# Performance work log

Hardware: AMD Instinct MI355X
Metric: run time of the kernel (lower is better)

Reference implementation:

```python
import jax, jax.numpy as jnp
import numpy as np

N = 50000      # nodes
E = 800000     # edges (before self-loops)
IN_F = 128     # in_feature
HID = 64       # hidden_feature (out_channels per head)
HEADS = 3
NEG_SLOPE = 0.2  # PyG GATConv default negative_slope


def setup_inputs() -> dict:
    key = jax.random.key(0)
    ks = jax.random.split(key, 12)
    x = jax.random.normal(ks[0], (N, IN_F), dtype=jnp.float32)
    src = jax.random.randint(ks[1], (E,), 0, N, dtype=jnp.int32)
    off = jax.random.randint(ks[2], (E,), 1, N, dtype=jnp.int32)
    dst = (src + off) % N  # guarantees no pre-existing self-loops
    edge_index = jnp.stack([src, dst]).astype(jnp.int32)

    def glorot(k, shape, fan_in):
        return (jax.random.normal(k, shape, dtype=jnp.float32)
                / np.float32(np.sqrt(fan_in)))

    W1 = glorot(ks[3], (IN_F, HEADS * HID), IN_F)
    att_src1 = glorot(ks[4], (HEADS, HID), HID)
    att_dst1 = glorot(ks[5], (HEADS, HID), HID)
    bias1 = jnp.zeros((HID,), jnp.float32)
    W2 = glorot(ks[6], (HID, HEADS * HID), HID)
    att_src2 = glorot(ks[7], (HEADS, HID), HID)
    att_dst2 = glorot(ks[8], (HEADS, HID), HID)
    bias2 = jnp.zeros((HID,), jnp.float32)
    return dict(x=x, edge_index=edge_index,
                W1=W1, att_src1=att_src1, att_dst1=att_dst1, bias1=bias1,
                W2=W2, att_src2=att_src2, att_dst2=att_dst2, bias2=bias2)


def gat_layer(x, W, a_src, a_dst, bias, src, dst):
    """PyG GATConv: heads=HEADS, concat=False (mean over heads), self-loops added."""
    h = (x @ W).reshape(-1, HEADS, HID)              # [N, H, C]
    alpha_src = jnp.einsum('nhc,hc->nh', h, a_src)   # [N, H]
    alpha_dst = jnp.einsum('nhc,hc->nh', h, a_dst)   # [N, H]
    loop = jnp.arange(N, dtype=src.dtype)
    s = jnp.concatenate([src, loop])                 # add self-loops
    d = jnp.concatenate([dst, loop])
    e = jax.nn.leaky_relu(alpha_src[s] + alpha_dst[d], NEG_SLOPE)  # [E+N, H]
    # segment softmax over edges grouped by destination node
    m = jax.ops.segment_max(e, d, num_segments=N)    # [N, H]; every node has a self-loop
    p = jnp.exp(e - m[d])
    denom = jax.ops.segment_sum(p, d, num_segments=N)
    alpha = p / (denom[d] + 1e-16)                   # [E+N, H]
    out = jax.ops.segment_sum(alpha[:, :, None] * h[s], d, num_segments=N)  # [N, H, C]
    return out.mean(axis=1) + bias                   # concat=False -> head mean


def reference(x, edge_index, W1, att_src1, att_dst1, bias1,
              W2, att_src2, att_dst2, bias2):
    src, dst = edge_index[0], edge_index[1]
    h1 = gat_layer(x, W1, att_src1, att_dst1, bias1, src, dst)
    h1 = jax.nn.relu(h1)  # dropout(p=0.2) is identity in eval mode
    return gat_layer(h1, W2, att_src2, att_dst2, bias2, src, dst)
```

## Files before the change

### kernel.cpp

```cpp
#include <hip/hip_runtime.h>
#include <hip/hip_fp16.h>
#include <math.h>
#include <limits.h>

#define N_NODES 50000
#define N_EDGES 800000
#define NEG 0.2f

typedef _Float16 half8 __attribute__((ext_vector_type(8)));
typedef float floatx4 __attribute__((ext_vector_type(4)));


__global__ void zero_kernel(int* a, int n) {
    int i = blockIdx.x * blockDim.x + threadIdx.x;
    if (i < n) a[i] = 0;
}

__global__ void count_kernel(const int* __restrict__ dst, int* cnt, int E) {
    int i = blockIdx.x * blockDim.x + threadIdx.x;
    if (i < E) atomicAdd(&cnt[dst[i]], 1);
}

__global__ void scan1_kernel(const int* __restrict__ cnt, int* rowptr, int* partials, int n) {
    __shared__ int sh[256];
    int tid = threadIdx.x;
    int i = blockIdx.x * 256 + tid;
    int v = (i < n) ? cnt[i] : 0;
    sh[tid] = v;
    __syncthreads();
    for (int off = 1; off < 256; off <<= 1) {
        int t = (tid >= off) ? sh[tid - off] : 0;
        __syncthreads();
        sh[tid] += t;
        __syncthreads();
    }
    if (i < n) rowptr[i] = sh[tid] - v;
    if (tid == 255) partials[blockIdx.x] = sh[255];
}

__global__ void scan2_kernel(int* partials, int nb) {
    __shared__ int sh[256];
    int tid = threadIdx.x;
    int v = (tid < nb) ? partials[tid] : 0;
    sh[tid] = v;
    __syncthreads();
    for (int off = 1; off < 256; off <<= 1) {
        int t = (tid >= off) ? sh[tid - off] : 0;
        __syncthreads();
        sh[tid] += t;
        __syncthreads();
    }
    if (tid < nb) partials[tid] = sh[tid] - v;
}

__global__ void scan3_kernel(int* rowptr, const int* __restrict__ partials, int n) {
    int i = blockIdx.x * blockDim.x + threadIdx.x;
    if (i < n) rowptr[i] += partials[i >> 8];
    if (i == 0) rowptr[n] = N_EDGES;
}

__global__ void fill_kernel(const int* __restrict__ src, const int* __restrict__ dst,
                            const int* __restrict__ rowptr, int* cnt, int* col, int* eidp, int E) {
    int i = blockIdx.x * blockDim.x + threadIdx.x;
    if (i < E) {
        int d = dst[i];
        int pos = rowptr[d] + atomicSub(&cnt[d], 1) - 1;
        col[pos] = src[i];
        eidp[pos] = i;
    }
}

__global__ void sortrow_kernel(const int* __restrict__ rowptr, int* col, int* eidp, int n) {
    int wid = (int)((blockIdx.x * blockDim.x + threadIdx.x) >> 6);
    int lane = threadIdx.x & 63;
    if (wid >= n) return;
    int r0 = rowptr[wid], r1 = rowptr[wid + 1];
    int deg = r1 - r0;
    if (deg <= 1) return;
    if (deg <= 64) {
        int key = (lane < deg) ? eidp[r0 + lane] : INT_MAX;
        int val = (lane < deg) ? col[r0 + lane] : 0;
#pragma unroll
        for (int k = 2; k <= 64; k <<= 1) {
#pragma unroll
            for (int j = k >> 1; j > 0; j >>= 1) {
                int pk = __shfl_xor(key, j);
                int pv = __shfl_xor(val, j);
                bool up = ((lane & k) == 0);
                bool lower = ((lane & j) == 0);
                bool take = lower ? ((pk < key) == up) : ((pk > key) == up);
                if (take) { key = pk; val = pv; }
            }
        }
        if (lane < deg) col[r0 + lane] = val;
    } else if (lane == 0) {
        for (int i = r0 + 1; i < r1; ++i) {
            int ke = eidp[i], kv = col[i];
            int j = i - 1;
            while (j >= r0 && eidp[j] > ke) {
                eidp[j + 1] = eidp[j];
                col[j + 1] = col[j];
                --j;
            }
            eidp[j + 1] = ke;
            col[j + 1] = kv;
        }
    }
}

template <int K>
__global__ void wtrans_kernel(const float* __restrict__ W, __half* __restrict__ wt) {
    int idx = blockIdx.x * blockDim.x + threadIdx.x;
    if (idx < 192 * K) {
        int n = idx / K, k = idx - n * K;
        wt[idx] = __float2half(W[k * 192 + n]);
    }
}

template <int K>
__global__ __launch_bounds__(256) void mfma_gemm_kernel(const float* __restrict__ A,
                                                        const __half* __restrict__ wt,
                                                        __half* __restrict__ out,
                                                        const float* __restrict__ att_src,
                                                        const float* __restrict__ att_dst,
                                                        float* __restrict__ as4,
                                                        float* __restrict__ ad4,
                                                        float* __restrict__ wself4, int rows) {
    constexpr int KP = K + 8;
    __shared__ __align__(16) __half lds[192 * KP];
    int tid = threadIdx.x;
    int lane = tid & 63;
    int wv = tid >> 6;
    int ln = lane & 15;
    int q = lane >> 4;

    for (int idx = tid; idx < 192 * (K / 8); idx += 256) {
        int n = idx / (K / 8), kk = (idx % (K / 8)) * 8;
        *(float4*)(lds + n * KP + kk) = *(const float4*)(wt + n * K + kk);
    }

    int m0 = blockIdx.x * 64 + wv * 16;
    int m = m0 + ln;
    int mc = m < rows ? m : 0;
    half8 afr[K / 32];
#pragma unroll
    for (int kt = 0; kt < K / 32; ++kt) {
        float4 a0 = *(const float4*)(A + (size_t)mc * K + kt * 32 + q * 8);
        float4 a1 = *(const float4*)(A + (size_t)mc * K + kt * 32 + q * 8 + 4);
        half8 f;
        f[0] = (_Float16)a0.x; f[1] = (_Float16)a0.y; f[2] = (_Float16)a0.z; f[3] = (_Float16)a0.w;
        f[4] = (_Float16)a1.x; f[5] = (_Float16)a1.y; f[6] = (_Float16)a1.z; f[7] = (_Float16)a1.w;
        afr[kt] = f;
    }

    __syncthreads();

    floatx4 acc[12];
#pragma unroll
    for (int c = 0; c < 12; ++c) acc[c] = (floatx4){0.f, 0.f, 0.f, 0.f};

#pragma unroll
    for (int kt = 0; kt < K / 32; ++kt) {
#pragma unroll
        for (int c = 0; c < 12; ++c) {
            half8 b = *(const half8*)(lds + (c * 16 + ln) * KP + kt * 32 + q * 8);
            acc[c] = __builtin_amdgcn_mfma_f32_16x16x32_f16(afr[kt], b, acc[c], 0, 0, 0);
        }
    }

    float asv[12], adv[12];
#pragma unroll
    for (int c = 0; c < 12; ++c) {
        asv[c] = att_src[c * 16 + ln];
        adv[c] = att_dst[c * 16 + ln];
    }
#pragma unroll
    for (int r = 0; r < 4; ++r) {
        float s0 = 0, s1 = 0, s2 = 0, d0 = 0, d1 = 0, d2 = 0;
#pragma unroll
        for (int c = 0; c < 4; ++c) { s0 += acc[c][r] * asv[c]; d0 += acc[c][r] * adv[c]; }
#pragma unroll
        for (int c = 4; c < 8; ++c) { s1 += acc[c][r] * asv[c]; d1 += acc[c][r] * adv[c]; }
#pragma unroll
        for (int c = 8; c < 12; ++c) { s2 += acc[c][r] * asv[c]; d2 += acc[c][r] * adv[c]; }
        for (int off = 1; off < 16; off <<= 1) {
            s0 += __shfl_xor(s0, off); s1 += __shfl_xor(s1, off); s2 += __shfl_xor(s2, off);
            d0 += __shfl_xor(d0, off); d1 += __shfl_xor(d1, off); d2 += __shfl_xor(d2, off);
        }
        int row = m0 + q * 4 + r;
        if (ln == 0 && row < rows) {
            as4[row * 4 + 0] = s0; as4[row * 4 + 1] = s1; as4[row * 4 + 2] = s2;
            ad4[row * 4 + 0] = d0; ad4[row * 4 + 1] = d1; ad4[row * 4 + 2] = d2;
            float v0 = s0 + d0; v0 = v0 > 0.f ? v0 : NEG * v0;
            float v1 = s1 + d1; v1 = v1 > 0.f ? v1 : NEG * v1;
            float v2 = s2 + d2; v2 = v2 > 0.f ? v2 : NEG * v2;
            wself4[row * 4 + 0] = __expf(v0);
            wself4[row * 4 + 1] = __expf(v1);
            wself4[row * 4 + 2] = __expf(v2);
        }
    }

    __syncthreads();
#pragma unroll
    for (int c = 0; c < 12; ++c)
#pragma unroll
        for (int r = 0; r < 4; ++r)
            lds[(wv * 16 + q * 4 + r) * 192 + c * 16 + ln] = __float2half(acc[c][r]);
    __syncthreads();
    int row0 = blockIdx.x * 64;
    for (int idx = tid; idx < 1536; idx += 256) {
        int row = (idx * 8) / 192, off = (idx * 8) % 192;
        if (row0 + row < rows)
            *(float4*)(out + (size_t)(row0 + row) * 192 + off) = *(float4*)(lds + row * 192 + off);
    }
}

template <bool RELU>
__global__ __launch_bounds__(256) void aggregate_kernel(const __half* __restrict__ h,
                                                        const float* __restrict__ as_,
                                                        const float* __restrict__ ad4,
                                                        const float* __restrict__ wself4,
                                                        const float* __restrict__ bias,
                                                        const int* __restrict__ rowptr,
                                                        const int* __restrict__ col,
                                                        float* __restrict__ out, int n) {
    constexpr int U = 8;
    __shared__ float sh[4][192];
    int wid = (int)((blockIdx.x * blockDim.x + threadIdx.x) >> 6);
    int l = threadIdx.x & 63;
    int wv = threadIdx.x >> 6;
    bool valid = wid < n;
    int d = valid ? wid : 0;
    if (valid && l < 48) {
        int hl = l >> 4;
        int r0 = rowptr[d], r1 = rowptr[d + 1];
        float adh = ad4[d * 4 + hl];
        float w = wself4[d * 4 + hl];
        float2 sraw = *(const float2*)(h + (size_t)d * 192 + l * 4);
        float2 s01 = __half22float2(*(__half2*)&sraw.x);
        float2 s23 = __half22float2(*(__half2*)&sraw.y);
        float ax = w * s01.x, ay = w * s01.y, az = w * s23.x, aw = w * s23.y;
        float den = w;

        for (int j = r0; j < r1; j += U) {
            int s[U];
            bool act[U];
            float av[U];
            float2 g[U];
#pragma unroll
            for (int u = 0; u < U; ++u) {
                int jj = j + u;
                act[u] = jj < r1;
                s[u] = act[u] ? col[jj] : 0;
            }
#pragma unroll
            for (int u = 0; u < U; ++u) {
                float t = as_[s[u] * 4 + hl];
                av[u] = act[u] ? t : -1e30f;
            }
#pragma unroll
            for (int u = 0; u < U; ++u)
                g[u] = *(const float2*)(h + (size_t)s[u] * 192 + l * 4);
#pragma unroll
            for (int u = 0; u < U; ++u) {
                float v = av[u] + adh;
                v = v > 0.f ? v : NEG * v;
                float we = __expf(v);
                float2 g01 = __half22float2(*(__half2*)&g[u].x);
                float2 g23 = __half22float2(*(__half2*)&g[u].y);
                den += we;
                ax += we * g01.x;
                ay += we * g01.y;
                az += we * g23.x;
                aw += we * g23.y;
            }
        }
        float r = 1.f / den;
        float4 o = {ax * r, ay * r, az * r, aw * r};
        *(float4*)&sh[wv][l * 4] = o;
    }
    __syncthreads();
    if (valid) {
        float o = (sh[wv][l] + sh[wv][64 + l] + sh[wv][128 + l]) * (1.f / 3.f) + bias[l];
        if (RELU) o = fmaxf(o, 0.f);
        out[(size_t)d * 64 + l] = o;
    }
}

extern "C" void kernel_launch(void* const* d_in, const int* in_sizes, int n_in,
                              void* d_out, int out_size, void* d_ws, size_t ws_size,
                              hipStream_t stream) {
    const float* x = (const float*)d_in[0];
    const int* ei = (const int*)d_in[1];
    const float* W1 = (const float*)d_in[2];
    const float* att_s1 = (const float*)d_in[3];
    const float* att_d1 = (const float*)d_in[4];
    const float* b1 = (const float*)d_in[5];
    const float* W2 = (const float*)d_in[6];
    const float* att_s2 = (const float*)d_in[7];
    const float* att_d2 = (const float*)d_in[8];
    const float* b2 = (const float*)d_in[9];
    const int* src = ei;
    const int* dst = ei + N_EDGES;

    __half* h16 = (__half*)d_ws;
    __half* wt1 = h16 + (size_t)N_NODES * 192;
    __half* wt2 = wt1 + 192 * 128;
    float* as4 = (float*)(wt2 + 192 * 64);
    float* ad4 = as4 + N_NODES * 4;
    float* wself4 = ad4 + N_NODES * 4;
    int* cnt = (int*)(wself4 + N_NODES * 4);
    int* rowptr = cnt + N_NODES;
    int* col = rowptr + N_NODES + 1;
    int* eidp = col + N_EDGES;
    int* partials = eidp + N_EDGES;

    float* outf = (float*)d_out;
    const int NB = (N_NODES + 255) / 256;

    wtrans_kernel<128><<<(192 * 128 + 255) / 256, 256, 0, stream>>>(W1, wt1);
    wtrans_kernel<64><<<(192 * 64 + 255) / 256, 256, 0, stream>>>(W2, wt2);

    zero_kernel<<<(N_NODES + 255) / 256, 256, 0, stream>>>(cnt, N_NODES);
    count_kernel<<<(N_EDGES + 255) / 256, 256, 0, stream>>>(dst, cnt, N_EDGES);
    scan1_kernel<<<NB, 256, 0, stream>>>(cnt, rowptr, partials, N_NODES);
    scan2_kernel<<<1, 256, 0, stream>>>(partials, NB);
    scan3_kernel<<<NB, 256, 0, stream>>>(rowptr, partials, N_NODES);
    fill_kernel<<<(N_EDGES + 255) / 256, 256, 0, stream>>>(src, dst, rowptr, cnt, col, eidp, N_EDGES);
    sortrow_kernel<<<(N_NODES + 3) / 4, 256, 0, stream>>>(rowptr, col, eidp, N_NODES);

    mfma_gemm_kernel<128><<<(N_NODES + 63) / 64, 256, 0, stream>>>(x, wt1, h16, att_s1, att_d1,
                                                                   as4, ad4, wself4, N_NODES);
    aggregate_kernel<true><<<(N_NODES + 3) / 4, 256, 0, stream>>>(h16, as4, ad4, wself4, b1,
                                                                  rowptr, col, outf, N_NODES);

    mfma_gemm_kernel<64><<<(N_NODES + 63) / 64, 256, 0, stream>>>(outf, wt2, h16, att_s2, att_d2,
                                                                  as4, ad4, wself4, N_NODES);
    aggregate_kernel<false><<<(N_NODES + 3) / 4, 256, 0, stream>>>(h16, as4, ad4, wself4, b2,
                                                                   rowptr, col, outf, N_NODES);
}
```

Measured before the change: 357.2 us.

## Streamline CSR build: store edge ids only, sort keys, then map to src

The CSR fill now writes only edge ids into col, using a cursor array that scan3 initializes, and the separate eidp array is dropped. The per-row bitonic sort then shuffles only keys and converts edge ids to source nodes at the end with a gathered load from src. Count and fill now process four edges per thread through int4 loads. This halves the scattered writes and shuffle traffic in the preprocessing stage, at the cost of an extra random gather from src during the sort.

```diff
diff --git a/kernel.cpp b/kernel.cpp
--- a/kernel.cpp
+++ b/kernel.cpp
@@ -17,8 +17,17 @@
 }
 
 __global__ void count_kernel(const int* __restrict__ dst, int* cnt, int E) {
-    int i = blockIdx.x * blockDim.x + threadIdx.x;
-    if (i < E) atomicAdd(&cnt[dst[i]], 1);
+    int t = blockIdx.x * blockDim.x + threadIdx.x;
+    int i0 = t * 4;
+    if (i0 + 3 < E) {
+        int4 d4 = *(const int4*)(dst + i0);
+        atomicAdd(&cnt[d4.x], 1);
+        atomicAdd(&cnt[d4.y], 1);
+        atomicAdd(&cnt[d4.z], 1);
+        atomicAdd(&cnt[d4.w], 1);
+    } else {
+        for (int i = i0; i < E; ++i) atomicAdd(&cnt[dst[i]], 1);
+    }
 }
 
 __global__ void scan1_kernel(const int* __restrict__ cnt, int* rowptr, int* partials, int n) {
@@ -53,58 +62,74 @@
     if (tid < nb) partials[tid] = sh[tid] - v;
 }
 
-__global__ void scan3_kernel(int* rowptr, const int* __restrict__ partials, int n) {
+__global__ void scan3_kernel(int* rowptr, const int* __restrict__ partials, int* cursor, int n) {
     int i = blockIdx.x * blockDim.x + threadIdx.x;
-    if (i < n) rowptr[i] += partials[i >> 8];
+    if (i < n) {
+        int v = rowptr[i] + partials[i >> 8];
+        rowptr[i] = v;
+        cursor[i] = v;
+    }
     if (i == 0) rowptr[n] = N_EDGES;
 }
 
-__global__ void fill_kernel(const int* __restrict__ src, const int* __restrict__ dst,
-                            const int* __restrict__ rowptr, int* cnt, int* col, int* eidp, int E) {
-    int i = blockIdx.x * blockDim.x + threadIdx.x;
-    if (i < E) {
-        int d = dst[i];
-        int pos = rowptr[d] + atomicSub(&cnt[d], 1) - 1;
-        col[pos] = src[i];
-        eidp[pos] = i;
-    }
-}
-
-__global__ void sortrow_kernel(const int* __restrict__ rowptr, int* col, int* eidp, int n) {
+__global__ void fill_kernel(const int* __restrict__ dst, int* cursor, int* col, int E) {
+    int t = blockIdx.x * blockDim.x + threadIdx.x;
+    int i0 = t * 4;
+    if (i0 + 3 < E) {
+        int4 d4 = *(const int4*)(dst + i0);
+        int p0 = atomicAdd(&cursor[d4.x], 1);
+        int p1 = atomicAdd(&cursor[d4.y], 1);
+        int p2 = atomicAdd(&cursor[d4.z], 1);
+        int p3 = atomicAdd(&cursor[d4.w], 1);
+        col[p0] = i0;
+        col[p1] = i0 + 1;
+        col[p2] = i0 + 2;
+        col[p3] = i0 + 3;
+    } else {
+        for (int i = i0; i < E; ++i) {
+            int p = atomicAdd(&cursor[dst[i]], 1);
+            col[p] = i;
+        }
+    }
+}
+
+__global__ void sortrow_kernel(const int* __restrict__ rowptr, int* col,
+                               const int* __restrict__ src, int n) {
     int wid = (int)((blockIdx.x * blockDim.x + threadIdx.x) >> 6);
     int lane = threadIdx.x & 63;
     if (wid >= n) return;
     int r0 = rowptr[wid], r1 = rowptr[wid + 1];
     int deg = r1 - r0;
-    if (deg <= 1) return;
+    if (deg <= 0) return;
+    if (deg == 1) {
+        if (lane == 0) col[r0] = src[col[r0]];
+        return;
+    }
     if (deg <= 64) {
-        int key = (lane < deg) ? eidp[r0 + lane] : INT_MAX;
-        int val = (lane < deg) ? col[r0 + lane] : 0;
+        int key = (lane < deg) ? col[r0 + lane] : INT_MAX;
 #pragma unroll
         for (int k = 2; k <= 64; k <<= 1) {
 #pragma unroll
             for (int j = k >> 1; j > 0; j >>= 1) {
                 int pk = __shfl_xor(key, j);
-                int pv = __shfl_xor(val, j);
                 bool up = ((lane & k) == 0);
                 bool lower = ((lane & j) == 0);
                 bool take = lower ? ((pk < key) == up) : ((pk > key) == up);
-                if (take) { key = pk; val = pv; }
-            }
-        }
-        if (lane < deg) col[r0 + lane] = val;
+                if (take) key = pk;
+            }
+        }
+        if (lane < deg) col[r0 + lane] = src[key];
     } else if (lane == 0) {
         for (int i = r0 + 1; i < r1; ++i) {
-            int ke = eidp[i], kv = col[i];
+            int kv = col[i];
             int j = i - 1;
-            while (j >= r0 && eidp[j] > ke) {
-                eidp[j + 1] = eidp[j];
+            while (j >= r0 && col[j] > kv) {
                 col[j + 1] = col[j];
                 --j;
             }
-            eidp[j + 1] = ke;
             col[j + 1] = kv;
         }
+        for (int i = r0; i < r1; ++i) col[i] = src[col[i]];
     }
 }
 
@@ -312,22 +337,22 @@
     int* cnt = (int*)(wself4 + N_NODES * 4);
     int* rowptr = cnt + N_NODES;
     int* col = rowptr + N_NODES + 1;
-    int* eidp = col + N_EDGES;
-    int* partials = eidp + N_EDGES;
+    int* partials = col + N_EDGES;
 
     float* outf = (float*)d_out;
     const int NB = (N_NODES + 255) / 256;
+    const int E4B = (N_EDGES / 4 + 255) / 256;
 
     wtrans_kernel<128><<<(192 * 128 + 255) / 256, 256, 0, stream>>>(W1, wt1);
     wtrans_kernel<64><<<(192 * 64 + 255) / 256, 256, 0, stream>>>(W2, wt2);
 
     zero_kernel<<<(N_NODES + 255) / 256, 256, 0, stream>>>(cnt, N_NODES);
-    count_kernel<<<(N_EDGES + 255) / 256, 256, 0, stream>>>(dst, cnt, N_EDGES);
+    count_kernel<<<E4B, 256, 0, stream>>>(dst, cnt, N_EDGES);
     scan1_kernel<<<NB, 256, 0, stream>>>(cnt, rowptr, partials, N_NODES);
     scan2_kernel<<<1, 256, 0, stream>>>(partials, NB);
-    scan3_kernel<<<NB, 256, 0, stream>>>(rowptr, partials, N_NODES);
-    fill_kernel<<<(N_EDGES + 255) / 256, 256, 0, stream>>>(src, dst, rowptr, cnt, col, eidp, N_EDGES);
-    sortrow_kernel<<<(N_NODES + 3) / 4, 256, 0, stream>>>(rowptr, col, eidp, N_NODES);
+    scan3_kernel<<<NB, 256, 0, stream>>>(rowptr, partials, cnt, N_NODES);
+    fill_kernel<<<E4B, 256, 0, stream>>>(dst, cnt, col, N_EDGES);
+    sortrow_kernel<<<(N_NODES + 3) / 4, 256, 0, stream>>>(rowptr, col, src, N_NODES);
 
     mfma_gemm_kernel<128><<<(N_NODES + 63) / 64, 256, 0, stream>>>(x, wt1, h16, att_s1, att_d1,
                                                                    as4, ad4, wself4, N_NODES);
```

Result: faster. 339.0 us (-5.1%).
